# Kernel optimization log

Measured on AMD Instinct MI355X. Metric: run time of the kernel, lower is better.

Reference implementation:

```python
import jax, jax.numpy as jnp
import numpy as np

N = 50000      # nodes
E = 800000     # edges (avg degree 16)
IN = 512       # input_dim
R = 128        # feat_reduce_dim
F = 64         # hid_dim per head
H = 4          # n_heads
OUT = 64       # output_dim
ALPHA = 0.2    # leaky_relu slope


def setup_inputs() -> dict:
    key = jax.random.key(0)
    ks = jax.random.split(key, 12)
    x = jax.random.normal(ks[0], (N, IN), dtype=jnp.float32)
    edges = jax.random.randint(ks[1], (2, E), 0, N, dtype=jnp.int32)
    # per-head GAT layer params (fan-in scaled so exp(logits) stays finite)
    W_lin_h = jax.random.normal(ks[2], (H, R, IN), dtype=jnp.float32) * (IN ** -0.5)
    W_seq_h = jax.random.normal(ks[3], (H, F, R), dtype=jnp.float32) * (R ** -0.5)
    a1_h = jax.random.normal(ks[4], (H, F), dtype=jnp.float32) * (F ** -0.5)
    b1_h = jnp.zeros((H,), dtype=jnp.float32)
    a2_h = jax.random.normal(ks[5], (H, F), dtype=jnp.float32) * (F ** -0.5)
    b2_h = jnp.zeros((H,), dtype=jnp.float32)
    bias_h = jnp.zeros((H, F), dtype=jnp.float32)
    # classifier GAT layer (in = H*F = 256, out = OUT)
    W_lin_c = jax.random.normal(ks[6], (R, H * F), dtype=jnp.float32) * ((H * F) ** -0.5)
    W_seq_c = jax.random.normal(ks[7], (OUT, R), dtype=jnp.float32) * (R ** -0.5)
    a1_c = jax.random.normal(ks[8], (OUT,), dtype=jnp.float32) * (OUT ** -0.5)
    b1_c = jnp.zeros((), dtype=jnp.float32)
    a2_c = jax.random.normal(ks[9], (OUT,), dtype=jnp.float32) * (OUT ** -0.5)
    b2_c = jnp.zeros((), dtype=jnp.float32)
    bias_c = jnp.zeros((OUT,), dtype=jnp.float32)
    return dict(x=x, edges=edges, W_lin_h=W_lin_h, W_seq_h=W_seq_h, a1_h=a1_h,
                b1_h=b1_h, a2_h=a2_h, b2_h=b2_h, bias_h=bias_h,
                W_lin_c=W_lin_c, W_seq_c=W_seq_c, a1_c=a1_c, b1_c=b1_c,
                a2_c=a2_c, b2_c=b2_c, bias_c=bias_c)


def _gat_layer(x, src, dst, W_lin, W_seq, a1, b1, a2, b2, bias, concat):
    n = x.shape[0]
    h = x @ W_lin.T                    # [N, R]   (Linear, no bias)
    s = h @ W_seq.T                    # [N, F]   (Conv1d k=1 == matmul)
    f1 = s @ a1 + b1                   # [N]      (f_1 conv)
    f2 = s @ a2 + b2                   # [N]      (f_2 conv)
    logits = f1[src] + f2[dst]         # [E]  edge-gather
    coefs = jnp.exp(jax.nn.leaky_relu(logits, ALPHA))          # [E]
    denom = jax.ops.segment_sum(coefs, src, num_segments=n)    # [N]
    agg = jax.ops.segment_sum(coefs[:, None] * s[dst], src, num_segments=n)  # [N, F]
    ret = agg / denom[:, None] + bias
    return jax.nn.elu(ret) if concat else ret


def reference(x, edges, W_lin_h, W_seq_h, a1_h, b1_h, a2_h, b2_h, bias_h,
              W_lin_c, W_seq_c, a1_c, b1_c, a2_c, b2_c, bias_c):
    src, dst = edges[0], edges[1]
    # n_heads attention layers (concat=True), vmapped over the head axis
    heads = jax.vmap(
        lambda Wl, Ws, a1, b1, a2, b2, b: _gat_layer(
            x, src, dst, Wl, Ws, a1, b1, a2, b2, b, True)
    )(W_lin_h, W_seq_h, a1_h, b1_h, a2_h, b2_h, bias_h)        # [H, N, F]
    hcat = jnp.transpose(heads, (1, 0, 2)).reshape(x.shape[0], -1)  # [N, H*F]
    # classifier GAT layer (concat=False -> no ELU)
    out = _gat_layer(hcat, src, dst, W_lin_c, W_seq_c, a1_c, b1_c,
                     a2_c, b2_c, bias_c, False)                # [N, OUT]
    return out
```

## Files before the change

kernel.cpp:

```cpp
#include <hip/hip_runtime.h>
#include <hip/hip_bf16.h>
#include <cstddef>
#include <cstdint>

#define IN_DIM 512
#define R_DIM 128
#define F_DIM 64
#define H_NUM 4
#define OUT_DIM 64
#define HF 256

typedef __attribute__((ext_vector_type(4))) float f32x4;
typedef __attribute__((ext_vector_type(8))) short bf16x8;

typedef const __attribute__((address_space(1))) void gas_void;
typedef __attribute__((address_space(3))) void las_void;

__device__ __forceinline__ float bf2f(ushort u) {
    union { uint i; float f; } v; v.i = ((uint)u) << 16; return v.f;
}
__device__ __forceinline__ ushort f2bf(float f) {
    union { float f; uint i; } v; v.f = f;
    uint r = v.i + 0x7fff + ((v.i >> 16) & 1);
    return (ushort)(r >> 16);
}
__device__ __forceinline__ float u2f(uint u) {
    union { uint i; float f; } v; v.i = u; return v.f;
}

__global__ __launch_bounds__(256) void zero_i32(int* __restrict__ p, int n) {
    int i = blockIdx.x * 256 + threadIdx.x;
    if (i < n) p[i] = 0;
}

__global__ __launch_bounds__(256) void wcomb1_kernel(const float* __restrict__ Wlin,
                                                     const float* __restrict__ Wseq,
                                                     ushort* __restrict__ Wc) {
    int idx = blockIdx.x * 256 + threadIdx.x;
    if (idx >= H_NUM * F_DIM * IN_DIM) return;
    int i  = idx & (IN_DIM - 1);
    int hf = idx >> 9;
    int h  = hf >> 6;
    const float* ws = Wseq + (size_t)hf * R_DIM;
    const float* wl = Wlin + (size_t)h * R_DIM * IN_DIM + i;
    float acc = 0.0f;
#pragma unroll 8
    for (int r = 0; r < R_DIM; ++r) acc += ws[r] * wl[(size_t)r * IN_DIM];
    Wc[idx] = f2bf(acc);
}

__global__ __launch_bounds__(256) void wcomb2_kernel(const float* __restrict__ Wlin,
                                                     const float* __restrict__ Wseq,
                                                     ushort* __restrict__ Wc) {
    int idx = blockIdx.x * 256 + threadIdx.x;
    if (idx >= OUT_DIM * HF) return;
    int j = idx & (HF - 1);
    int o = idx >> 8;
    const float* ws = Wseq + (size_t)o * R_DIM;
    const float* wl = Wlin + j;
    float acc = 0.0f;
#pragma unroll 8
    for (int r = 0; r < R_DIM; ++r) acc += ws[r] * wl[(size_t)r * HF];
    Wc[idx] = f2bf(acc);
}

template<int BN, int K, int FS>
__global__ __launch_bounds__(256) void gemm_f32a(const float* __restrict__ A,
                                                 const ushort* __restrict__ B,
                                                 ushort* __restrict__ C,
                                                 int M, int Ntot,
                                                 const float* __restrict__ a1,
                                                 const float* __restrict__ b1,
                                                 const float* __restrict__ a2,
                                                 const float* __restrict__ b2,
                                                 float* __restrict__ f1o,
                                                 float* __restrict__ f2o) {
    constexpr int NF = BN / 16;
    constexpr int HH = BN / 64;
    __shared__ ushort As[64 * 64];
    __shared__ ushort Bs[BN * 64];
    const int tid = threadIdx.x;
    const int wave = tid >> 6;
    const int lane = tid & 63;
    const int lr = lane & 15;
    const int lg = lane >> 4;
    const int m0 = blockIdx.x * 64;

    int base[2];
#pragma unroll
    for (int ks = 0; ks < 2; ++ks)
        base[ks] = lr * 128 + (((ks * 4 + lg) ^ (lr & 7)) * 16);
    const int abase0 = wave * 2048 + base[0];
    const int abase1 = wave * 2048 + base[1];

    f32x4 acc[NF];
#pragma unroll
    for (int cb = 0; cb < NF; ++cb) acc[cb] = (f32x4)0.0f;

    for (int k0 = 0; k0 < K; k0 += 64) {
#pragma unroll
        for (int r = 0; r < BN / 32; ++r) {
            int off = r * 4096 + tid * 16;
            int row = off >> 7;
            int kch = ((off >> 4) & 7) ^ (row & 7);
            const ushort* g = B + (size_t)row * K + k0 + kch * 8;
            __builtin_amdgcn_global_load_lds((gas_void*)g,
                                             (las_void*)((char*)Bs + off), 16, 0, 0);
        }
#pragma unroll
        for (int r = 0; r < 2; ++r) {
            int off = r * 4096 + tid * 16;
            int row = off >> 7;
            int grow = m0 + row;
            if (grow >= M) grow = M - 1;
            int lchunk = (off >> 4) & 7;
            const float* g = A + (size_t)grow * K + k0 + lchunk * 8;
            float4 v0 = *(const float4*)(g);
            float4 v1 = *(const float4*)(g + 4);
            ushort us[8] = {f2bf(v0.x), f2bf(v0.y), f2bf(v0.z), f2bf(v0.w),
                            f2bf(v1.x), f2bf(v1.y), f2bf(v1.z), f2bf(v1.w)};
            int ldsoff = row * 128 + ((lchunk ^ (row & 7)) * 16);
            *(uint4*)((char*)As + ldsoff) = *(const uint4*)us;
        }
        __syncthreads();
        {
            bf16x8 af0 = *(const bf16x8*)((const char*)As + abase0);
            bf16x8 af1 = *(const bf16x8*)((const char*)As + abase1);
#pragma unroll
            for (int cg = 0; cg < NF / 4; ++cg) {
                bf16x8 bfr[4];
#pragma unroll
                for (int j = 0; j < 4; ++j)
                    bfr[j] = *(const bf16x8*)((const char*)Bs + (cg * 4 + j) * 2048 + base[0]);
#pragma unroll
                for (int j = 0; j < 4; ++j)
                    acc[cg * 4 + j] = __builtin_amdgcn_mfma_f32_16x16x32_bf16(
                        af0, bfr[j], acc[cg * 4 + j], 0, 0, 0);
#pragma unroll
                for (int j = 0; j < 4; ++j)
                    bfr[j] = *(const bf16x8*)((const char*)Bs + (cg * 4 + j) * 2048 + base[1]);
#pragma unroll
                for (int j = 0; j < 4; ++j)
                    acc[cg * 4 + j] = __builtin_amdgcn_mfma_f32_16x16x32_bf16(
                        af1, bfr[j], acc[cg * 4 + j], 0, 0, 0);
            }
        }
        __syncthreads();
    }

    float a1v[NF], a2v[NF];
#pragma unroll
    for (int cb = 0; cb < NF; ++cb) {
        int col = cb * 16 + lr;
        a1v[cb] = a1[col];
        a2v[cb] = a2[col];
    }
    const int rowb = m0 + wave * 16 + lg * 4;
#pragma unroll
    for (int r = 0; r < 4; ++r) {
        int row = rowb + r;
        bool ok = row < M;
#pragma unroll
        for (int hh = 0; hh < HH; ++hh) {
            float p1 = 0.f, p2 = 0.f;
#pragma unroll
            for (int c4 = 0; c4 < 4; ++c4) {
                int cb = hh * 4 + c4;
                float v = acc[cb][r];
                p1 += v * a1v[cb];
                p2 += v * a2v[cb];
                if (ok) C[(size_t)row * Ntot + cb * 16 + lr] = f2bf(v);
            }
#pragma unroll
            for (int m = 1; m < 16; m <<= 1) {
                p1 += __shfl_xor(p1, m, 64);
                p2 += __shfl_xor(p2, m, 64);
            }
            if (lr == 0 && ok) {
                f1o[(size_t)row * FS + hh] = p1 + b1[hh];
                f2o[(size_t)row * FS + hh] = p2 + b2[hh];
            }
        }
    }
}

template<int BN, int K, int FS>
__global__ __launch_bounds__(256) void gemm_bf16(const ushort* __restrict__ A,
                                                 const ushort* __restrict__ B,
                                                 ushort* __restrict__ C,
                                                 int M, int Ntot,
                                                 const float* __restrict__ a1,
                                                 const float* __restrict__ b1,
                                                 const float* __restrict__ a2,
                                                 const float* __restrict__ b2,
                                                 float* __restrict__ f1o,
                                                 float* __restrict__ f2o) {
    constexpr int NF = BN / 16;
    constexpr int HH = BN / 64;
    __shared__ ushort As[64 * 64];
    __shared__ ushort Bs[BN * 64];
    const int tid = threadIdx.x;
    const int wave = tid >> 6;
    const int lane = tid & 63;
    const int lr = lane & 15;
    const int lg = lane >> 4;
    const int m0 = blockIdx.x * 64;

    int base[2];
#pragma unroll
    for (int ks = 0; ks < 2; ++ks)
        base[ks] = lr * 128 + (((ks * 4 + lg) ^ (lr & 7)) * 16);
    const int abase0 = wave * 2048 + base[0];
    const int abase1 = wave * 2048 + base[1];

    f32x4 acc[NF];
#pragma unroll
    for (int cb = 0; cb < NF; ++cb) acc[cb] = (f32x4)0.0f;

    for (int k0 = 0; k0 < K; k0 += 64) {
#pragma unroll
        for (int r = 0; r < 2; ++r) {
            int off = r * 4096 + tid * 16;
            int row = off >> 7;
            int kch = ((off >> 4) & 7) ^ (row & 7);
            const ushort* g = A + (size_t)(m0 + row) * K + k0 + kch * 8;
            __builtin_amdgcn_global_load_lds((gas_void*)g,
                                             (las_void*)((char*)As + off), 16, 0, 0);
        }
#pragma unroll
        for (int r = 0; r < BN / 32; ++r) {
            int off = r * 4096 + tid * 16;
            int row = off >> 7;
            int kch = ((off >> 4) & 7) ^ (row & 7);
            const ushort* g = B + (size_t)row * K + k0 + kch * 8;
            __builtin_amdgcn_global_load_lds((gas_void*)g,
                                             (las_void*)((char*)Bs + off), 16, 0, 0);
        }
        __syncthreads();
        {
            bf16x8 af0 = *(const bf16x8*)((const char*)As + abase0);
            bf16x8 af1 = *(const bf16x8*)((const char*)As + abase1);
#pragma unroll
            for (int cg = 0; cg < NF / 4; ++cg) {
                bf16x8 bfr[4];
#pragma unroll
                for (int j = 0; j < 4; ++j)
                    bfr[j] = *(const bf16x8*)((const char*)Bs + (cg * 4 + j) * 2048 + base[0]);
#pragma unroll
                for (int j = 0; j < 4; ++j)
                    acc[cg * 4 + j] = __builtin_amdgcn_mfma_f32_16x16x32_bf16(
                        af0, bfr[j], acc[cg * 4 + j], 0, 0, 0);
#pragma unroll
                for (int j = 0; j < 4; ++j)
                    bfr[j] = *(const bf16x8*)((const char*)Bs + (cg * 4 + j) * 2048 + base[1]);
#pragma unroll
                for (int j = 0; j < 4; ++j)
                    acc[cg * 4 + j] = __builtin_amdgcn_mfma_f32_16x16x32_bf16(
                        af1, bfr[j], acc[cg * 4 + j], 0, 0, 0);
            }
        }
        __syncthreads();
    }

    float a1v[NF], a2v[NF];
#pragma unroll
    for (int cb = 0; cb < NF; ++cb) {
        int col = cb * 16 + lr;
        a1v[cb] = a1[col];
        a2v[cb] = a2[col];
    }
    const int rowb = m0 + wave * 16 + lg * 4;
#pragma unroll
    for (int r = 0; r < 4; ++r) {
        int row = rowb + r;
        bool ok = row < M;
#pragma unroll
        for (int hh = 0; hh < HH; ++hh) {
            float p1 = 0.f, p2 = 0.f;
#pragma unroll
            for (int c4 = 0; c4 < 4; ++c4) {
                int cb = hh * 4 + c4;
                float v = acc[cb][r];
                p1 += v * a1v[cb];
                p2 += v * a2v[cb];
                if (ok) C[(size_t)row * Ntot + cb * 16 + lr] = f2bf(v);
            }
#pragma unroll
            for (int m = 1; m < 16; m <<= 1) {
                p1 += __shfl_xor(p1, m, 64);
                p2 += __shfl_xor(p2, m, 64);
            }
            if (lr == 0 && ok) {
                f1o[(size_t)row * FS + hh] = p1 + b1[hh];
                f2o[(size_t)row * FS + hh] = p2 + b2[hh];
            }
        }
    }
}

__global__ __launch_bounds__(256) void hist_kernel(const int* __restrict__ src,
                                                   int* __restrict__ counts, int E) {
    int e = blockIdx.x * 256 + threadIdx.x;
    if (e < E) atomicAdd(&counts[src[e]], 1);
}

__global__ __launch_bounds__(256) void scan_blk(const int* __restrict__ counts,
                                                int* __restrict__ lexcl,
                                                int* __restrict__ part, int N) {
    __shared__ int wsum[4];
    int t = threadIdx.x;
    int g = blockIdx.x * 256 + t;
    int lane = t & 63, wid = t >> 6;
    int v = (g < N) ? counts[g] : 0;
    int x = v;
#pragma unroll
    for (int off = 1; off < 64; off <<= 1) {
        int u = __shfl_up(x, off, 64);
        if (lane >= off) x += u;
    }
    if (lane == 63) wsum[wid] = x;
    __syncthreads();
    int woff = 0;
#pragma unroll
    for (int w = 0; w < 3; ++w) if (w < wid) woff += wsum[w];
    int incl = x + woff;
    if (g < N) lexcl[g] = incl - v;
    if (t == 255) part[blockIdx.x] = incl;
}

__global__ __launch_bounds__(256) void scan_part(int* __restrict__ part, int nb) {
    __shared__ int wsum[4];
    int t = threadIdx.x;
    int lane = t & 63, wid = t >> 6;
    int v = (t < nb) ? part[t] : 0;
    int x = v;
#pragma unroll
    for (int off = 1; off < 64; off <<= 1) {
        int u = __shfl_up(x, off, 64);
        if (lane >= off) x += u;
    }
    if (lane == 63) wsum[wid] = x;
    __syncthreads();
    int woff = 0;
#pragma unroll
    for (int w = 0; w < 3; ++w) if (w < wid) woff += wsum[w];
    int incl = x + woff;
    __syncthreads();
    if (t < nb) part[t] = incl - v;
    if (t == 255) part[nb] = incl;
}

__global__ __launch_bounds__(256) void scan_add(const int* __restrict__ lexcl,
                                                const int* __restrict__ part,
                                                int* __restrict__ starts,
                                                int* __restrict__ cursor, int N, int nb) {
    int g = blockIdx.x * 256 + threadIdx.x;
    if (g < N) {
        int s = lexcl[g] + part[blockIdx.x];
        starts[g] = s;
        cursor[g] = s;
    }
    if (g == 0) starts[N] = part[nb];
}

__global__ __launch_bounds__(256) void scatter_kernel(const int* __restrict__ src,
                                                      const int* __restrict__ dst,
                                                      int* __restrict__ cursor,
                                                      int* __restrict__ dsts, int E) {
    int e = blockIdx.x * 256 + threadIdx.x;
    if (e >= E) return;
    int p = atomicAdd(&cursor[src[e]], 1);
    dsts[p] = dst[e];
}

__global__ __launch_bounds__(256) void gather1_kernel(const int* __restrict__ starts,
                                                      const int* __restrict__ dsts,
                                                      const float* __restrict__ f1,
                                                      const float* __restrict__ f2,
                                                      const ushort* __restrict__ S1,
                                                      const float* __restrict__ bias,
                                                      ushort* __restrict__ hcat, int N) {
    int n = (int)((blockIdx.x * blockDim.x + threadIdx.x) >> 6);
    int lane = threadIdx.x & 63;
    if (n >= N) return;
    const int head = lane >> 4;
    const float f1h = f1[(size_t)n * 4 + head];
    int beg = starts[n], end = starts[n + 1];
    float a0 = 0.f, a1 = 0.f, a2 = 0.f, a3 = 0.f, den = 0.f;
    int i = beg;
    for (; i + 4 <= end; i += 4) {
        int4 d4 = *(const int4*)(dsts + i);
        float g0 = f2[(size_t)d4.x * 4 + head];
        float g1 = f2[(size_t)d4.y * 4 + head];
        float g2 = f2[(size_t)d4.z * 4 + head];
        float g3 = f2[(size_t)d4.w * 4 + head];
        uint2 r0 = *(const uint2*)(S1 + (size_t)d4.x * HF + lane * 4);
        uint2 r1 = *(const uint2*)(S1 + (size_t)d4.y * HF + lane * 4);
        uint2 r2 = *(const uint2*)(S1 + (size_t)d4.z * HF + lane * 4);
        uint2 r3 = *(const uint2*)(S1 + (size_t)d4.w * HF + lane * 4);
        float l0 = f1h + g0; l0 = l0 > 0.f ? l0 : 0.2f * l0;
        float l1 = f1h + g1; l1 = l1 > 0.f ? l1 : 0.2f * l1;
        float l2 = f1h + g2; l2 = l2 > 0.f ? l2 : 0.2f * l2;
        float l3 = f1h + g3; l3 = l3 > 0.f ? l3 : 0.2f * l3;
        float c0 = __expf(l0), c1 = __expf(l1), c2 = __expf(l2), c3 = __expf(l3);
        a0 += c0 * u2f(r0.x << 16);        a1 += c0 * u2f(r0.x & 0xffff0000u);
        a2 += c0 * u2f(r0.y << 16);        a3 += c0 * u2f(r0.y & 0xffff0000u);
        a0 += c1 * u2f(r1.x << 16);        a1 += c1 * u2f(r1.x & 0xffff0000u);
        a2 += c1 * u2f(r1.y << 16);        a3 += c1 * u2f(r1.y & 0xffff0000u);
        a0 += c2 * u2f(r2.x << 16);        a1 += c2 * u2f(r2.x & 0xffff0000u);
        a2 += c2 * u2f(r2.y << 16);        a3 += c2 * u2f(r2.y & 0xffff0000u);
        a0 += c3 * u2f(r3.x << 16);        a1 += c3 * u2f(r3.x & 0xffff0000u);
        a2 += c3 * u2f(r3.y << 16);        a3 += c3 * u2f(r3.y & 0xffff0000u);
        den += c0 + c1 + c2 + c3;
    }
    for (; i < end; ++i) {
        int d = dsts[i];
        float g = f2[(size_t)d * 4 + head];
        uint2 r = *(const uint2*)(S1 + (size_t)d * HF + lane * 4);
        float l = f1h + g; l = l > 0.f ? l : 0.2f * l;
        float c = __expf(l);
        a0 += c * u2f(r.x << 16);  a1 += c * u2f(r.x & 0xffff0000u);
        a2 += c * u2f(r.y << 16);  a3 += c * u2f(r.y & 0xffff0000u);
        den += c;
    }
    float rd = __builtin_amdgcn_rcpf(den);
    float4 b = *(const float4*)(bias + lane * 4);
    float v0 = a0 * rd + b.x;
    float v1 = a1 * rd + b.y;
    float v2 = a2 * rd + b.z;
    float v3 = a3 * rd + b.w;
    v0 = v0 > 0.f ? v0 : __expf(v0) - 1.f;
    v1 = v1 > 0.f ? v1 : __expf(v1) - 1.f;
    v2 = v2 > 0.f ? v2 : __expf(v2) - 1.f;
    v3 = v3 > 0.f ? v3 : __expf(v3) - 1.f;
    ushort4 o;
    o.x = f2bf(v0); o.y = f2bf(v1); o.z = f2bf(v2); o.w = f2bf(v3);
    *(ushort4*)(hcat + (size_t)n * HF + lane * 4) = o;
}

__global__ __launch_bounds__(256) void gather2_kernel(const int* __restrict__ starts,
                                                      const int* __restrict__ dsts,
                                                      const float* __restrict__ f1,
                                                      const float* __restrict__ f2,
                                                      const ushort* __restrict__ S2,
                                                      const float* __restrict__ bias,
                                                      float* __restrict__ out, int N) {
    int n = (int)((blockIdx.x * blockDim.x + threadIdx.x) >> 6);
    int lane = threadIdx.x & 63;
    if (n >= N) return;
    const float f1u = f1[n];
    int beg = starts[n], end = starts[n + 1];
    float acc = 0.f, den = 0.f;
    int i = beg;
    for (; i + 4 <= end; i += 4) {
        int4 d4 = *(const int4*)(dsts + i);
        float g0 = f2[d4.x], g1 = f2[d4.y], g2 = f2[d4.z], g3 = f2[d4.w];
        ushort r0 = S2[(size_t)d4.x * OUT_DIM + lane];
        ushort r1 = S2[(size_t)d4.y * OUT_DIM + lane];
        ushort r2 = S2[(size_t)d4.z * OUT_DIM + lane];
        ushort r3 = S2[(size_t)d4.w * OUT_DIM + lane];
        float l0 = f1u + g0; l0 = l0 > 0.f ? l0 : 0.2f * l0;
        float l1 = f1u + g1; l1 = l1 > 0.f ? l1 : 0.2f * l1;
        float l2 = f1u + g2; l2 = l2 > 0.f ? l2 : 0.2f * l2;
        float l3 = f1u + g3; l3 = l3 > 0.f ? l3 : 0.2f * l3;
        float c0 = __expf(l0), c1 = __expf(l1), c2 = __expf(l2), c3 = __expf(l3);
        acc += c0 * bf2f(r0) + c1 * bf2f(r1) + c2 * bf2f(r2) + c3 * bf2f(r3);
        den += c0 + c1 + c2 + c3;
    }
    for (; i < end; ++i) {
        int d = dsts[i];
        float l = f1u + f2[d]; l = l > 0.f ? l : 0.2f * l;
        float c = __expf(l);
        acc += c * bf2f(S2[(size_t)d * OUT_DIM + lane]);
        den += c;
    }
    out[(size_t)n * OUT_DIM + lane] = acc * __builtin_amdgcn_rcpf(den) + bias[lane];
}

extern "C" void kernel_launch(void* const* d_in, const int* in_sizes, int n_in,
                              void* d_out, int out_size, void* d_ws, size_t ws_size,
                              hipStream_t stream) {
    const float* x      = (const float*)d_in[0];
    const int*   edges  = (const int*)d_in[1];
    const float* Wlin_h = (const float*)d_in[2];
    const float* Wseq_h = (const float*)d_in[3];
    const float* a1_h   = (const float*)d_in[4];
    const float* b1_h   = (const float*)d_in[5];
    const float* a2_h   = (const float*)d_in[6];
    const float* b2_h   = (const float*)d_in[7];
    const float* bias_h = (const float*)d_in[8];
    const float* Wlin_c = (const float*)d_in[9];
    const float* Wseq_c = (const float*)d_in[10];
    const float* a1_c   = (const float*)d_in[11];
    const float* b1_c   = (const float*)d_in[12];
    const float* a2_c   = (const float*)d_in[13];
    const float* b2_c   = (const float*)d_in[14];
    const float* bias_c = (const float*)d_in[15];

    const int N = in_sizes[0] / IN_DIM;
    const int E = in_sizes[1] / 2;
    const int* src = edges;
    const int* dst = edges + E;

    char* ws = (char*)d_ws;
    size_t off = 0;
    ushort* WC1   = (ushort*)(ws + off); off += (size_t)HF * IN_DIM * 2;
    ushort* WC2   = (ushort*)(ws + off); off += (size_t)OUT_DIM * HF * 2;
    ushort* S1    = (ushort*)(ws + off); off += (size_t)N * HF * 2;
    ushort* S2    = S1;
    ushort* HCAT  = (ushort*)(ws + off); off += (size_t)N * HF * 2;
    float*  F1    = (float*)(ws + off);  off += (size_t)N * H_NUM * 4;
    float*  F2    = (float*)(ws + off);  off += (size_t)N * H_NUM * 4;
    float*  F1c   = (float*)(ws + off);  off += (size_t)N * 4;
    float*  F2c   = (float*)(ws + off);  off += (size_t)N * 4;
    int* COUNTS   = (int*)(ws + off);    off += (size_t)N * 4;
    int* STARTS   = (int*)(ws + off);    off += ((size_t)N + 1) * 4;
    int* CURSOR   = (int*)(ws + off);    off += (size_t)N * 4;
    int* DSTS     = (int*)(ws + off);    off += (size_t)E * 4;
    int* LEXCL    = (int*)(ws + off);    off += (size_t)N * 4;
    int* PART     = (int*)(ws + off);    off += 512 * 4;

    float* out = (float*)d_out;

    const int eg = (E + 255) / 256;
    const int NB = (N + 255) / 256;

    hipLaunchKernelGGL(zero_i32, dim3(NB), dim3(256), 0, stream, COUNTS, N);
    hipLaunchKernelGGL(hist_kernel, dim3(eg), dim3(256), 0, stream, src, COUNTS, E);
    hipLaunchKernelGGL(scan_blk, dim3(NB), dim3(256), 0, stream, COUNTS, LEXCL, PART, N);
    hipLaunchKernelGGL(scan_part, dim3(1), dim3(256), 0, stream, PART, NB);
    hipLaunchKernelGGL(scan_add, dim3(NB), dim3(256), 0, stream, LEXCL, PART, STARTS, CURSOR, N, NB);
    hipLaunchKernelGGL(scatter_kernel, dim3(eg), dim3(256), 0, stream, src, dst, CURSOR, DSTS, E);

    hipLaunchKernelGGL(wcomb1_kernel, dim3((HF * IN_DIM + 255) / 256), dim3(256),
                       0, stream, Wlin_h, Wseq_h, WC1);
    hipLaunchKernelGGL(wcomb2_kernel, dim3((OUT_DIM * HF + 255) / 256), dim3(256),
                       0, stream, Wlin_c, Wseq_c, WC2);

    hipLaunchKernelGGL((gemm_f32a<HF, IN_DIM, 4>), dim3((N + 63) / 64, 1), dim3(256),
                       0, stream, x, WC1, S1, N, HF,
                       a1_h, b1_h, a2_h, b2_h, F1, F2);

    hipLaunchKernelGGL(gather1_kernel, dim3((N + 3) / 4), dim3(256), 0, stream,
                       STARTS, DSTS, F1, F2, S1, bias_h, HCAT, N);

    hipLaunchKernelGGL((gemm_bf16<OUT_DIM, HF, 1>), dim3((N + 63) / 64, 1), dim3(256),
                       0, stream, HCAT, WC2, S2, N, OUT_DIM,
                       a1_c, b1_c, a2_c, b2_c, F1c, F2c);

    hipLaunchKernelGGL(gather2_kernel, dim3((N + 3) / 4), dim3(256), 0, stream,
                       STARTS, DSTS, F1c, F2c, S2, bias_c, out, N);
}
```

Baseline: 268.7 us.

## Split head GEMM across column halves and rework gathers to two edges per wave

The first GEMM now uses a 128-column tile with a 2D grid that is swizzled so both column halves of the same row block run on neighbouring blocks, aiming at more occupancy and L2 reuse of the fp32 x rows. Both gather kernels split each wave into two half-waves that each process a different edge using wider vector loads, then combine the halves with a cross-lane shuffle. The two weight-combine kernels are merged into a single launch. The cost is that x is read and converted to bf16 twice (once per column half), the tail edges are unbalanced across the half-waves, and the shuffle reduction adds a little work.

```diff
diff --git a/kernel.cpp b/kernel.cpp
--- a/kernel.cpp
+++ b/kernel.cpp
@@ -33,35 +33,35 @@
     if (i < n) p[i] = 0;
 }
 
-__global__ __launch_bounds__(256) void wcomb1_kernel(const float* __restrict__ Wlin,
-                                                     const float* __restrict__ Wseq,
-                                                     ushort* __restrict__ Wc) {
+__global__ __launch_bounds__(256) void wcomb_kernel(const float* __restrict__ WlinH,
+                                                    const float* __restrict__ WseqH,
+                                                    const float* __restrict__ WlinC,
+                                                    const float* __restrict__ WseqC,
+                                                    ushort* __restrict__ Wc1,
+                                                    ushort* __restrict__ Wc2) {
     int idx = blockIdx.x * 256 + threadIdx.x;
-    if (idx >= H_NUM * F_DIM * IN_DIM) return;
-    int i  = idx & (IN_DIM - 1);
-    int hf = idx >> 9;
-    int h  = hf >> 6;
-    const float* ws = Wseq + (size_t)hf * R_DIM;
-    const float* wl = Wlin + (size_t)h * R_DIM * IN_DIM + i;
-    float acc = 0.0f;
+    if (idx < H_NUM * F_DIM * IN_DIM) {
+        int i  = idx & (IN_DIM - 1);
+        int hf = idx >> 9;
+        int h  = hf >> 6;
+        const float* ws = WseqH + (size_t)hf * R_DIM;
+        const float* wl = WlinH + (size_t)h * R_DIM * IN_DIM + i;
+        float acc = 0.0f;
 #pragma unroll 8
-    for (int r = 0; r < R_DIM; ++r) acc += ws[r] * wl[(size_t)r * IN_DIM];
-    Wc[idx] = f2bf(acc);
-}
-
-__global__ __launch_bounds__(256) void wcomb2_kernel(const float* __restrict__ Wlin,
-                                                     const float* __restrict__ Wseq,
-                                                     ushort* __restrict__ Wc) {
-    int idx = blockIdx.x * 256 + threadIdx.x;
-    if (idx >= OUT_DIM * HF) return;
-    int j = idx & (HF - 1);
-    int o = idx >> 8;
-    const float* ws = Wseq + (size_t)o * R_DIM;
-    const float* wl = Wlin + j;
-    float acc = 0.0f;
+        for (int r = 0; r < R_DIM; ++r) acc += ws[r] * wl[(size_t)r * IN_DIM];
+        Wc1[idx] = f2bf(acc);
+    } else {
+        int idx2 = idx - H_NUM * F_DIM * IN_DIM;
+        if (idx2 >= OUT_DIM * HF) return;
+        int j = idx2 & (HF - 1);
+        int o = idx2 >> 8;
+        const float* ws = WseqC + (size_t)o * R_DIM;
+        const float* wl = WlinC + j;
+        float acc = 0.0f;
 #pragma unroll 8
-    for (int r = 0; r < R_DIM; ++r) acc += ws[r] * wl[(size_t)r * HF];
-    Wc[idx] = f2bf(acc);
+        for (int r = 0; r < R_DIM; ++r) acc += ws[r] * wl[(size_t)r * HF];
+        Wc2[idx2] = f2bf(acc);
+    }
 }
 
 template<int BN, int K, int FS>
@@ -84,7 +84,15 @@
     const int lane = tid & 63;
     const int lr = lane & 15;
     const int lg = lane >> 4;
-    const int m0 = blockIdx.x * 64;
+
+    const int b = blockIdx.x;
+    const int by = (b >> 3) & 1;
+    const int bx = (b >> 4) * 8 + (b & 7);
+    const int nbx = (M + 63) >> 6;
+    if (bx >= nbx) return;
+    const int m0 = bx * 64;
+    const int n0 = by * BN;
+    const int h0 = by * HH;
 
     int base[2];
 #pragma unroll
@@ -93,6 +101,19 @@
     const int abase0 = wave * 2048 + base[0];
     const int abase1 = wave * 2048 + base[1];
 
+    int s_grow[2], s_ldsoff[2], s_goff[2];
+#pragma unroll
+    for (int r = 0; r < 2; ++r) {
+        int off = r * 4096 + tid * 16;
+        int row = off >> 7;
+        int lchunk = (off >> 4) & 7;
+        int grow = m0 + row;
+        if (grow >= M) grow = M - 1;
+        s_grow[r] = grow;
+        s_goff[r] = lchunk * 8;
+        s_ldsoff[r] = row * 128 + ((lchunk ^ (row & 7)) * 16);
+    }
+
     f32x4 acc[NF];
 #pragma unroll
     for (int cb = 0; cb < NF; ++cb) acc[cb] = (f32x4)0.0f;
@@ -103,24 +124,18 @@
             int off = r * 4096 + tid * 16;
             int row = off >> 7;
             int kch = ((off >> 4) & 7) ^ (row & 7);
-            const ushort* g = B + (size_t)row * K + k0 + kch * 8;
+            const ushort* g = B + (size_t)(n0 + row) * K + k0 + kch * 8;
             __builtin_amdgcn_global_load_lds((gas_void*)g,
                                              (las_void*)((char*)Bs + off), 16, 0, 0);
         }
 #pragma unroll
         for (int r = 0; r < 2; ++r) {
-            int off = r * 4096 + tid * 16;
-            int row = off >> 7;
-            int grow = m0 + row;
-            if (grow >= M) grow = M - 1;
-            int lchunk = (off >> 4) & 7;
-            const float* g = A + (size_t)grow * K + k0 + lchunk * 8;
+            const float* g = A + (size_t)s_grow[r] * K + k0 + s_goff[r];
             float4 v0 = *(const float4*)(g);
             float4 v1 = *(const float4*)(g + 4);
             ushort us[8] = {f2bf(v0.x), f2bf(v0.y), f2bf(v0.z), f2bf(v0.w),
                             f2bf(v1.x), f2bf(v1.y), f2bf(v1.z), f2bf(v1.w)};
-            int ldsoff = row * 128 + ((lchunk ^ (row & 7)) * 16);
-            *(uint4*)((char*)As + ldsoff) = *(const uint4*)us;
+            *(uint4*)((char*)As + s_ldsoff[r]) = *(const uint4*)us;
         }
         __syncthreads();
         {
@@ -151,7 +166,7 @@
     float a1v[NF], a2v[NF];
 #pragma unroll
     for (int cb = 0; cb < NF; ++cb) {
-        int col = cb * 16 + lr;
+        int col = n0 + cb * 16 + lr;
         a1v[cb] = a1[col];
         a2v[cb] = a2[col];
     }
@@ -169,7 +184,7 @@
                 float v = acc[cb][r];
                 p1 += v * a1v[cb];
                 p2 += v * a2v[cb];
-                if (ok) C[(size_t)row * Ntot + cb * 16 + lr] = f2bf(v);
+                if (ok) C[(size_t)row * Ntot + n0 + cb * 16 + lr] = f2bf(v);
             }
 #pragma unroll
             for (int m = 1; m < 16; m <<= 1) {
@@ -177,8 +192,8 @@
                 p2 += __shfl_xor(p2, m, 64);
             }
             if (lr == 0 && ok) {
-                f1o[(size_t)row * FS + hh] = p1 + b1[hh];
-                f2o[(size_t)row * FS + hh] = p2 + b2[hh];
+                f1o[(size_t)row * FS + h0 + hh] = p1 + b1[h0 + hh];
+                f2o[(size_t)row * FS + h0 + hh] = p2 + b2[h0 + hh];
             }
         }
     }
@@ -383,59 +398,66 @@
     int n = (int)((blockIdx.x * blockDim.x + threadIdx.x) >> 6);
     int lane = threadIdx.x & 63;
     if (n >= N) return;
-    const int head = lane >> 4;
+    const int es = lane >> 5;
+    const int fl = lane & 31;
+    const int head = fl >> 3;
     const float f1h = f1[(size_t)n * 4 + head];
     int beg = starts[n], end = starts[n + 1];
-    float a0 = 0.f, a1 = 0.f, a2 = 0.f, a3 = 0.f, den = 0.f;
+    float a[8] = {};
+    float den = 0.f;
     int i = beg;
+
+#define G1_EDGE(D)                                                            \
+    {                                                                         \
+        float g_ = f2[(size_t)(D) * 4 + head];                                \
+        uint4 r_ = *(const uint4*)(S1 + (size_t)(D) * HF + fl * 8);           \
+        float l_ = f1h + g_; l_ = l_ > 0.f ? l_ : 0.2f * l_;                  \
+        float c_ = __expf(l_);                                                \
+        a[0] += c_ * u2f(r_.x << 16);  a[1] += c_ * u2f(r_.x & 0xffff0000u);  \
+        a[2] += c_ * u2f(r_.y << 16);  a[3] += c_ * u2f(r_.y & 0xffff0000u);  \
+        a[4] += c_ * u2f(r_.z << 16);  a[5] += c_ * u2f(r_.z & 0xffff0000u);  \
+        a[6] += c_ * u2f(r_.w << 16);  a[7] += c_ * u2f(r_.w & 0xffff0000u);  \
+        den += c_;                                                            \
+    }
+
     for (; i + 4 <= end; i += 4) {
-        int4 d4 = *(const int4*)(dsts + i);
-        float g0 = f2[(size_t)d4.x * 4 + head];
-        float g1 = f2[(size_t)d4.y * 4 + head];
-        float g2 = f2[(size_t)d4.z * 4 + head];
-        float g3 = f2[(size_t)d4.w * 4 + head];
-        uint2 r0 = *(const uint2*)(S1 + (size_t)d4.x * HF + lane * 4);
-        uint2 r1 = *(const uint2*)(S1 + (size_t)d4.y * HF + lane * 4);
-        uint2 r2 = *(const uint2*)(S1 + (size_t)d4.z * HF + lane * 4);
-        uint2 r3 = *(const uint2*)(S1 + (size_t)d4.w * HF + lane * 4);
-        float l0 = f1h + g0; l0 = l0 > 0.f ? l0 : 0.2f * l0;
-        float l1 = f1h + g1; l1 = l1 > 0.f ? l1 : 0.2f * l1;
-        float l2 = f1h + g2; l2 = l2 > 0.f ? l2 : 0.2f * l2;
-        float l3 = f1h + g3; l3 = l3 > 0.f ? l3 : 0.2f * l3;
-        float c0 = __expf(l0), c1 = __expf(l1), c2 = __expf(l2), c3 = __expf(l3);
-        a0 += c0 * u2f(r0.x << 16);        a1 += c0 * u2f(r0.x & 0xffff0000u);
-        a2 += c0 * u2f(r0.y << 16);        a3 += c0 * u2f(r0.y & 0xffff0000u);
-        a0 += c1 * u2f(r1.x << 16);        a1 += c1 * u2f(r1.x & 0xffff0000u);
-        a2 += c1 * u2f(r1.y << 16);        a3 += c1 * u2f(r1.y & 0xffff0000u);
-        a0 += c2 * u2f(r2.x << 16);        a1 += c2 * u2f(r2.x & 0xffff0000u);
-        a2 += c2 * u2f(r2.y << 16);        a3 += c2 * u2f(r2.y & 0xffff0000u);
-        a0 += c3 * u2f(r3.x << 16);        a1 += c3 * u2f(r3.x & 0xffff0000u);
-        a2 += c3 * u2f(r3.y << 16);        a3 += c3 * u2f(r3.y & 0xffff0000u);
-        den += c0 + c1 + c2 + c3;
-    }
-    for (; i < end; ++i) {
+        int dA = dsts[i + es];
+        int dB = dsts[i + 2 + es];
+        G1_EDGE(dA);
+        G1_EDGE(dB);
+    }
+    if (i + 2 <= end) {
+        int d = dsts[i + es];
+        G1_EDGE(d);
+        i += 2;
+    }
+    if (i < end && es == 0) {
         int d = dsts[i];
-        float g = f2[(size_t)d * 4 + head];
-        uint2 r = *(const uint2*)(S1 + (size_t)d * HF + lane * 4);
-        float l = f1h + g; l = l > 0.f ? l : 0.2f * l;
-        float c = __expf(l);
-        a0 += c * u2f(r.x << 16);  a1 += c * u2f(r.x & 0xffff0000u);
-        a2 += c * u2f(r.y << 16);  a3 += c * u2f(r.y & 0xffff0000u);
-        den += c;
-    }
-    float rd = __builtin_amdgcn_rcpf(den);
-    float4 b = *(const float4*)(bias + lane * 4);
-    float v0 = a0 * rd + b.x;
-    float v1 = a1 * rd + b.y;
-    float v2 = a2 * rd + b.z;
-    float v3 = a3 * rd + b.w;
-    v0 = v0 > 0.f ? v0 : __expf(v0) - 1.f;
-    v1 = v1 > 0.f ? v1 : __expf(v1) - 1.f;
-    v2 = v2 > 0.f ? v2 : __expf(v2) - 1.f;
-    v3 = v3 > 0.f ? v3 : __expf(v3) - 1.f;
-    ushort4 o;
-    o.x = f2bf(v0); o.y = f2bf(v1); o.z = f2bf(v2); o.w = f2bf(v3);
-    *(ushort4*)(hcat + (size_t)n * HF + lane * 4) = o;
+        G1_EDGE(d);
+    }
+#undef G1_EDGE
+
+#pragma unroll
+    for (int k = 0; k < 8; ++k) a[k] += __shfl_xor(a[k], 32, 64);
+    den += __shfl_xor(den, 32, 64);
+
+    if (es == 0) {
+        float rd = __builtin_amdgcn_rcpf(den);
+        float4 b0 = *(const float4*)(bias + fl * 8);
+        float4 b1 = *(const float4*)(bias + fl * 8 + 4);
+        float v[8];
+        v[0] = a[0] * rd + b0.x; v[1] = a[1] * rd + b0.y;
+        v[2] = a[2] * rd + b0.z; v[3] = a[3] * rd + b0.w;
+        v[4] = a[4] * rd + b1.x; v[5] = a[5] * rd + b1.y;
+        v[6] = a[6] * rd + b1.z; v[7] = a[7] * rd + b1.w;
+        ushort us[8];
+#pragma unroll
+        for (int k = 0; k < 8; ++k) {
+            float vv = v[k] > 0.f ? v[k] : __expf(v[k]) - 1.f;
+            us[k] = f2bf(vv);
+        }
+        *(uint4*)(hcat + (size_t)n * HF + fl * 8) = *(const uint4*)us;
+    }
 }
 
 __global__ __launch_bounds__(256) void gather2_kernel(const int* __restrict__ starts,
@@ -448,33 +470,53 @@
     int n = (int)((blockIdx.x * blockDim.x + threadIdx.x) >> 6);
     int lane = threadIdx.x & 63;
     if (n >= N) return;
+    const int es = lane >> 5;
+    const int fl = lane & 31;
     const float f1u = f1[n];
     int beg = starts[n], end = starts[n + 1];
-    float acc = 0.f, den = 0.f;
+    float a0 = 0.f, a1 = 0.f, den = 0.f;
     int i = beg;
+
+#define G2_EDGE(D)                                                            \
+    {                                                                         \
+        float g_ = f2[(D)];                                                   \
+        uint r_ = *(const uint*)(S2 + (size_t)(D) * OUT_DIM + fl * 2);        \
+        float l_ = f1u + g_; l_ = l_ > 0.f ? l_ : 0.2f * l_;                  \
+        float c_ = __expf(l_);                                                \
+        a0 += c_ * u2f(r_ << 16);                                             \
+        a1 += c_ * u2f(r_ & 0xffff0000u);                                     \
+        den += c_;                                                            \
+    }
+
     for (; i + 4 <= end; i += 4) {
-        int4 d4 = *(const int4*)(dsts + i);
-        float g0 = f2[d4.x], g1 = f2[d4.y], g2 = f2[d4.z], g3 = f2[d4.w];
-        ushort r0 = S2[(size_t)d4.x * OUT_DIM + lane];
-        ushort r1 = S2[(size_t)d4.y * OUT_DIM + lane];
-        ushort r2 = S2[(size_t)d4.z * OUT_DIM + lane];
-        ushort r3 = S2[(size_t)d4.w * OUT_DIM + lane];
-        float l0 = f1u + g0; l0 = l0 > 0.f ? l0 : 0.2f * l0;
-        float l1 = f1u + g1; l1 = l1 > 0.f ? l1 : 0.2f * l1;
-        float l2 = f1u + g2; l2 = l2 > 0.f ? l2 : 0.2f * l2;
-        float l3 = f1u + g3; l3 = l3 > 0.f ? l3 : 0.2f * l3;
-        float c0 = __expf(l0), c1 = __expf(l1), c2 = __expf(l2), c3 = __expf(l3);
-        acc += c0 * bf2f(r0) + c1 * bf2f(r1) + c2 * bf2f(r2) + c3 * bf2f(r3);
-        den += c0 + c1 + c2 + c3;
-    }
-    for (; i < end; ++i) {
+        int dA = dsts[i + es];
+        int dB = dsts[i + 2 + es];
+        G2_EDGE(dA);
+        G2_EDGE(dB);
+    }
+    if (i + 2 <= end) {
+        int d = dsts[i + es];
+        G2_EDGE(d);
+        i += 2;
+    }
+    if (i < end && es == 0) {
         int d = dsts[i];
-        float l = f1u + f2[d]; l = l > 0.f ? l : 0.2f * l;
-        float c = __expf(l);
-        acc += c * bf2f(S2[(size_t)d * OUT_DIM + lane]);
-        den += c;
-    }
-    out[(size_t)n * OUT_DIM + lane] = acc * __builtin_amdgcn_rcpf(den) + bias[lane];
+        G2_EDGE(d);
+    }
+#undef G2_EDGE
+
+    a0 += __shfl_xor(a0, 32, 64);
+    a1 += __shfl_xor(a1, 32, 64);
+    den += __shfl_xor(den, 32, 64);
+
+    if (es == 0) {
+        float rd = __builtin_amdgcn_rcpf(den);
+        float2 b = *(const float2*)(bias + fl * 2);
+        float2 o;
+        o.x = a0 * rd + b.x;
+        o.y = a1 * rd + b.y;
+        *(float2*)(out + (size_t)n * OUT_DIM + fl * 2) = o;
+    }
 }
 
 extern "C" void kernel_launch(void* const* d_in, const int* in_sizes, int n_in,
@@ -532,14 +574,17 @@
     hipLaunchKernelGGL(scan_add, dim3(NB), dim3(256), 0, stream, LEXCL, PART, STARTS, CURSOR, N, NB);
     hipLaunchKernelGGL(scatter_kernel, dim3(eg), dim3(256), 0, stream, src, dst, CURSOR, DSTS, E);
 
-    hipLaunchKernelGGL(wcomb1_kernel, dim3((HF * IN_DIM + 255) / 256), dim3(256),
-                       0, stream, Wlin_h, Wseq_h, WC1);
-    hipLaunchKernelGGL(wcomb2_kernel, dim3((OUT_DIM * HF + 255) / 256), dim3(256),
-                       0, stream, Wlin_c, Wseq_c, WC2);
-
-    hipLaunchKernelGGL((gemm_f32a<HF, IN_DIM, 4>), dim3((N + 63) / 64, 1), dim3(256),
-                       0, stream, x, WC1, S1, N, HF,
-                       a1_h, b1_h, a2_h, b2_h, F1, F2);
+    hipLaunchKernelGGL(wcomb_kernel,
+                       dim3((H_NUM * F_DIM * IN_DIM + OUT_DIM * HF + 255) / 256), dim3(256),
+                       0, stream, Wlin_h, Wseq_h, Wlin_c, Wseq_c, WC1, WC2);
+
+    {
+        int nbx = (N + 63) / 64;
+        int gx = 16 * ((nbx + 7) / 8);
+        hipLaunchKernelGGL((gemm_f32a<128, IN_DIM, 4>), dim3(gx), dim3(256),
+                           0, stream, x, WC1, S1, N, HF,
+                           a1_h, b1_h, a2_h, b2_h, F1, F2);
+    }
 
     hipLaunchKernelGGL(gather1_kernel, dim3((N + 3) / 4), dim3(256), 0, stream,
                        STARTS, DSTS, F1, F2, S1, bias_h, HCAT, N);
```

After: 248.1 us. -7.7%, faster.
